# Kernel optimization log

Hardware: AMD Instinct MI355X
Metric: run time of the kernel (lower is better)

The kernel has to match this reference:

```python
import jax, jax.numpy as jnp
import numpy as np

HEADS = 4
F_OUT = 64
NEG_SLOPE = 0.2


def setup_inputs() -> dict:
    key = jax.random.key(0)
    k1, k2, k3, k4 = jax.random.split(key, 4)
    N, F_IN = 4096, 256
    x = jax.random.normal(k1, (N, F_IN), dtype=jnp.float32)
    adj = jax.random.randint(k2, (N, N), 0, 2, dtype=jnp.int32)
    # nn.Linear stores weight [out, in]; we store transposed [in, out] for x @ W
    W = jax.random.normal(k3, (F_IN, F_OUT * HEADS), dtype=jnp.float32) * (1.0 / np.sqrt(F_IN))
    a = jax.random.normal(k4, (2 * F_OUT, 1), dtype=jnp.float32) * 0.1
    return {"x": x, "adj": adj, "W": W, "a": a}


def reference(x, adj, W, a):
    N = x.shape[0]
    h = (x @ W).reshape(N, HEADS, F_OUT)              # [N, H, F]
    # matmul(cat(h_i, h_j), a) == h_i @ a1 + h_j @ a2 (exact, avoids O(N^2*2F) h_cat)
    a1 = a[:F_OUT, 0]
    a2 = a[F_OUT:, 0]
    e_i = jnp.einsum('nhf,f->nh', h, a1)              # [N, H]
    e_j = jnp.einsum('nhf,f->nh', h, a2)              # [N, H]
    e = e_i[:, None, :] + e_j[None, :, :]             # [N, N, H]
    e = jnp.where(e > 0, e, NEG_SLOPE * e)            # LeakyReLU(0.2)
    e = jnp.where(adj[:, :, None] == 0, -jnp.inf, e)
    attention = jax.nn.softmax(e, axis=1)             # softmax over source nodes j
    h_prime = jnp.einsum('ijh,jhf->ihf', attention, h)  # [N, H, F]
    return h_prime.mean(axis=1)                       # heads > 1 -> mean over heads
```

## Files before the change

kernel.cpp:

```cpp
#include <hip/hip_runtime.h>

#define N     4096
#define FIN   256
#define CC    256
#define HEADS 4
#define FOUT  64
#define XPITCH 266

typedef __attribute__((ext_vector_type(8))) short bf16x8;
typedef __attribute__((ext_vector_type(4))) float f32x4;
typedef __attribute__((ext_vector_type(2))) float f32x2;

__device__ inline unsigned cvtpk(float lo, float hi) {
    unsigned r;
    asm("v_cvt_pk_bf16_f32 %0, %1, %2" : "=v"(r) : "v"(lo), "v"(hi));
    return r;
}
__device__ inline f32x2 pkmul(f32x2 a, f32x2 b) {
    f32x2 r;
    asm("v_pk_mul_f32 %0, %1, %2" : "=v"(r) : "v"(a), "v"(b));
    return r;
}

__global__ __launch_bounds__(512) void gat_k1a(const float* __restrict__ x,
                                               const float* __restrict__ W,
                                               const float* __restrict__ a,
                                               short* __restrict__ hF,
                                               float2* __restrict__ e1f,
                                               float2* __restrict__ e2f) {
    __shared__ __align__(16) short xs[64][XPITCH];
    __shared__ __align__(16) short wts[64][XPITCH];
    __shared__ __align__(16) short hbuf[64][74];
    const int t    = threadIdx.x;
    const int bid  = blockIdx.x;
    const int lane = t & 63;
    const int w    = t >> 6;

    const int hd = bid >> 6;
    const int n0 = (bid & 63) * 64;
    const int c0 = hd * 64;

    {
        const float4* xsrc = (const float4*)(x + (size_t)n0 * FIN);
        #pragma unroll
        for (int it = 0; it < 8; ++it) {
            const int fi = it * 512 + t;
            const float4 v = xsrc[fi];
            uint2 o;
            o.x = cvtpk(v.x, v.y);
            o.y = cvtpk(v.z, v.w);
            *(uint2*)&xs[fi >> 6][(fi & 63) * 4] = o;
        }
    }
    {
        const int c  = t & 63;
        const int k4 = (t >> 6) * 4;
        #pragma unroll
        for (int it = 0; it < 8; ++it) {
            const int k = it * 32 + k4;
            const float w0 = W[(k + 0) * CC + c0 + c];
            const float w1 = W[(k + 1) * CC + c0 + c];
            const float w2 = W[(k + 2) * CC + c0 + c];
            const float w3 = W[(k + 3) * CC + c0 + c];
            uint2 o;
            o.x = cvtpk(w0, w1);
            o.y = cvtpk(w2, w3);
            *(uint2*)&wts[c][k] = o;
        }
    }
    __syncthreads();

    const int m = lane & 15;
    const int q = lane >> 4;

    if (w < 4) {
        f32x4 acc[4];
        #pragma unroll
        for (int ct = 0; ct < 4; ++ct) acc[ct] = (f32x4){0.f, 0.f, 0.f, 0.f};

        #pragma unroll
        for (int ks = 0; ks < 8; ++ks) {
            const bf16x8 af = *(const bf16x8*)&xs[w * 16 + m][ks * 32 + q * 8];
            #pragma unroll
            for (int ct = 0; ct < 4; ++ct) {
                const bf16x8 bf_ = *(const bf16x8*)&wts[ct * 16 + m][ks * 32 + q * 8];
                acc[ct] = __builtin_amdgcn_mfma_f32_16x16x32_bf16(af, bf_, acc[ct], 0, 0, 0);
            }
        }

        const float a1v[4] = {a[m], a[16 + m], a[32 + m], a[48 + m]};
        const float a2v[4] = {a[64 + m], a[80 + m], a[96 + m], a[112 + m]};
        #pragma unroll
        for (int r = 0; r < 4; ++r) {
            float s1 = 0.f, s2 = 0.f;
            #pragma unroll
            for (int ct = 0; ct < 4; ++ct) {
                s1 = fmaf(acc[ct][r], a1v[ct], s1);
                s2 = fmaf(acc[ct][r], a2v[ct], s2);
            }
            #pragma unroll
            for (int sh = 1; sh < 16; sh <<= 1) {
                s1 += __shfl_xor(s1, sh, 64);
                s2 += __shfl_xor(s2, sh, 64);
            }
            if (m == 0) {
                const int n = n0 + w * 16 + q * 4 + r;
                e1f[(size_t)hd * N + n] = make_float2(__expf(s1), __expf(0.2f * s1));
                e2f[(size_t)hd * N + n] = make_float2(__expf(s2), __expf(0.2f * s2));
            }
        }

        #pragma unroll
        for (int ct = 0; ct < 4; ++ct) {
            const unsigned lo = cvtpk(acc[ct][0], acc[ct][1]);
            const unsigned hi = cvtpk(acc[ct][2], acc[ct][3]);
            unsigned* hp = (unsigned*)&hbuf[ct * 16 + m][w * 16 + q * 4];
            hp[0] = lo;
            hp[1] = hi;
        }
    }
    __syncthreads();

    {
        const int lp = t & 63;
        const int ft = (t >> 6) & 3;
        const int c2 = t >> 8;
        const int mm = lp & 15;
        const int qq = lp >> 4;
        const bf16x8 hv = *(const bf16x8*)&hbuf[ft * 16 + mm][c2 * 32 + qq * 8];
        const size_t jc = (size_t)(n0 >> 5) + c2;
        *(bf16x8*)(hF + ((((size_t)hd * 128 + jc) * 4 + ft) * 64 + lp) * 8) = hv;
    }
}

__global__ __launch_bounds__(256) void gat_k1b(const int* __restrict__ adj,
                                               unsigned* __restrict__ adjb) {
    const int t    = threadIdx.x;
    const int lane = t & 63;
    const int w    = t >> 6;
    const int row  = blockIdx.x * 2 + (w >> 1);
    const int half = w & 1;
    const int4* arow4 = (const int4*)(adj + (size_t)row * N) + half * 512;
    unsigned*   drow  = adjb + (size_t)row * 128 + half * 64;

    int4 ca[8];
    #pragma unroll
    for (int k = 0; k < 8; ++k)
        ca[k] = arow4[k * 64 + lane];
    #pragma unroll
    for (int k = 0; k < 8; ++k) {
        const int4 v = ca[k];
        unsigned n = (v.x != 0 ? 1u : 0u) | (v.y != 0 ? 2u : 0u) |
                     (v.z != 0 ? 4u : 0u) | (v.w != 0 ? 8u : 0u);
        unsigned b  = n   | ((unsigned)__shfl_xor((int)n,   1, 64) << 4);
        unsigned hw = b   | ((unsigned)__shfl_xor((int)b,   2, 64) << 8);
        unsigned d  = hw  | ((unsigned)__shfl_xor((int)hw,  4, 64) << 16);
        if ((lane & 7) == 0) drow[k * 8 + (lane >> 3)] = d;
    }
}

__global__ __launch_bounds__(512, 4) void gat_k2b(const short* __restrict__ hF,
                                                  const unsigned* __restrict__ adjb,
                                                  const float2* __restrict__ e1f,
                                                  const float2* __restrict__ e2f,
                                                  float* __restrict__ num,
                                                  float* __restrict__ Zp) {
    __shared__ __align__(16) short    hstage[2][4096];
    __shared__ __align__(16) float    e2s[2048];
    __shared__ __align__(16) unsigned adjl[128 * 36];
    __shared__ __align__(16) uint4    mtab[256];
    const int t    = threadIdx.x;
    const int lane = t & 63;
    const int g    = t >> 6;
    const int bid  = blockIdx.x;
    const int xcd  = bid & 7;
    const int idx  = bid >> 3;
    const int hd   = idx & 3;
    const int jc   = (idx >> 2) & 3;
    const int it   = xcd | ((idx >> 4) << 3);
    const int i0   = it * 128;
    const int j0   = jc * 1024;
    const int m    = lane & 15;
    const int q    = lane >> 4;
    const int slice = hd * 4 + jc;

    ((float4*)e2s)[t] = ((const float4*)(e2f + (size_t)hd * N + j0))[t];
    {
        const int row = t >> 2, part = t & 3;
        const uint4* src = (const uint4*)(adjb + (size_t)(i0 + row) * 128 + jc * 32 + part * 8);
        uint4* dst = (uint4*)(adjl + row * 36 + part * 8);
        dst[0] = src[0];
        dst[1] = src[1];
    }
    if (t < 256) {
        const unsigned b = t;
        uint4 e;
        e.x = ((b & 1u)   ? 0xFFFFu : 0u) | ((b & 2u)   ? 0xFFFF0000u : 0u);
        e.y = ((b & 4u)   ? 0xFFFFu : 0u) | ((b & 8u)   ? 0xFFFF0000u : 0u);
        e.z = ((b & 16u)  ? 0xFFFFu : 0u) | ((b & 32u)  ? 0xFFFF0000u : 0u);
        e.w = ((b & 64u)  ? 0xFFFFu : 0u) | ((b & 128u) ? 0xFFFF0000u : 0u);
        mtab[b] = e;
    }
    const uint4* gsrc = (const uint4*)(hF + ((size_t)hd * 128 + jc * 32) * 2048);
    ((uint4*)hstage[0])[t] = gsrc[t];
    __syncthreads();

    const int    rowi = i0 + g * 16 + m;
    const float2 E1r  = e1f[(size_t)hd * N + rowi];
    const f32x2  E1pk = (f32x2){E1r.x, E1r.y};

    bf16x8 onesb;
    #pragma unroll
    for (int e = 0; e < 8; ++e) onesb[e] = (short)0x3F80;

    f32x4 acc[4];
    #pragma unroll
    for (int ft = 0; ft < 4; ++ft) acc[ft] = (f32x4){0.f, 0.f, 0.f, 0.f};
    f32x4 accz = (f32x4){0.f, 0.f, 0.f, 0.f};

    const unsigned char* ab = ((const unsigned char*)adjl) + (g * 16 + m) * 144 + q;

    int cur = 0;
    #pragma unroll 2
    for (int mac = 0; mac < 16; ++mac) {
        const uint4 v = gsrc[(size_t)((mac + 1) & 15) * 512 + t];

        const unsigned bits0 = (unsigned)ab[(mac * 2 + 0) * 4];
        const unsigned bits1 = (unsigned)ab[(mac * 2 + 1) * 4];
        const uint4 mk0 = mtab[bits0];
        const uint4 mk1 = mtab[bits1];

        const short* hb = &hstage[cur][0];
        #pragma unroll
        for (int s = 0; s < 2; ++s) {
            const int jloc = mac * 64 + s * 32 + q * 8;
            const bf16x8 b0 = *(const bf16x8*)(hb + s * 2048 + 0 * 512 + lane * 8);
            const bf16x8 b1 = *(const bf16x8*)(hb + s * 2048 + 1 * 512 + lane * 8);
            const bf16x8 b2 = *(const bf16x8*)(hb + s * 2048 + 2 * 512 + lane * 8);
            const bf16x8 b3 = *(const bf16x8*)(hb + s * 2048 + 3 * 512 + lane * 8);
            const float4* ev = (const float4*)&e2s[2 * jloc];
            const float4 d0 = ev[0], d1 = ev[1], d2 = ev[2], d3 = ev[3];
            const uint4 mk = s ? mk1 : mk0;

            const f32x2 p0 = pkmul(E1pk, (f32x2){d0.x, d0.y});
            const f32x2 p1 = pkmul(E1pk, (f32x2){d0.z, d0.w});
            const f32x2 p2 = pkmul(E1pk, (f32x2){d1.x, d1.y});
            const f32x2 p3 = pkmul(E1pk, (f32x2){d1.z, d1.w});
            const f32x2 p4 = pkmul(E1pk, (f32x2){d2.x, d2.y});
            const f32x2 p5 = pkmul(E1pk, (f32x2){d2.z, d2.w});
            const f32x2 p6 = pkmul(E1pk, (f32x2){d3.x, d3.y});
            const f32x2 p7 = pkmul(E1pk, (f32x2){d3.z, d3.w});

            uint4 afu;
            afu.x = cvtpk(fmaxf(p0[0], p0[1]), fmaxf(p1[0], p1[1])) & mk.x;
            afu.y = cvtpk(fmaxf(p2[0], p2[1]), fmaxf(p3[0], p3[1])) & mk.y;
            afu.z = cvtpk(fmaxf(p4[0], p4[1]), fmaxf(p5[0], p5[1])) & mk.z;
            afu.w = cvtpk(fmaxf(p6[0], p6[1]), fmaxf(p7[0], p7[1])) & mk.w;
            const bf16x8 af = __builtin_bit_cast(bf16x8, afu);

            acc[0] = __builtin_amdgcn_mfma_f32_16x16x32_bf16(af, b0, acc[0], 0, 0, 0);
            acc[1] = __builtin_amdgcn_mfma_f32_16x16x32_bf16(af, b1, acc[1], 0, 0, 0);
            acc[2] = __builtin_amdgcn_mfma_f32_16x16x32_bf16(af, b2, acc[2], 0, 0, 0);
            acc[3] = __builtin_amdgcn_mfma_f32_16x16x32_bf16(af, b3, acc[3], 0, 0, 0);
            accz   = __builtin_amdgcn_mfma_f32_16x16x32_bf16(af, onesb, accz, 0, 0, 0);
        }

        if (mac < 15) {
            ((uint4*)hstage[cur ^ 1])[t] = v;
            __syncthreads();
            cur ^= 1;
        }
    }

    if (m == 0) {
        #pragma unroll
        for (int r = 0; r < 4; ++r)
            Zp[(size_t)slice * N + i0 + g * 16 + q * 4 + r] = accz[r];
    }

    {
        float* nrow = num + ((size_t)slice * N + i0 + g * 16) * FOUT;
        #pragma unroll
        for (int ft = 0; ft < 4; ++ft)
            #pragma unroll
            for (int r = 0; r < 4; ++r)
                nrow[(q * 4 + r) * FOUT + ft * 16 + m] = acc[ft][r];
    }
}

__global__ __launch_bounds__(256) void gat_k3(const float* __restrict__ num,
                                              const float* __restrict__ Zp,
                                              float* __restrict__ out) {
    const int g4 = blockIdx.x * 256 + threadIdx.x;
    const int i  = g4 >> 4;
    const int fo = (g4 & 15) * 4;
    float4 r = make_float4(0.f, 0.f, 0.f, 0.f);
    #pragma unroll
    for (int hd = 0; hd < 4; ++hd) {
        float4 s = make_float4(0.f, 0.f, 0.f, 0.f);
        float  z = 0.f;
        #pragma unroll
        for (int jc = 0; jc < 4; ++jc) {
            const int sl = hd * 4 + jc;
            const float4 v = *(const float4*)(num + ((size_t)sl * N + i) * FOUT + fo);
            s.x += v.x; s.y += v.y; s.z += v.z; s.w += v.w;
            z += Zp[(size_t)sl * N + i];
        }
        const float inv = 1.f / z;
        r.x += s.x * inv; r.y += s.y * inv; r.z += s.z * inv; r.w += s.w * inv;
    }
    r.x *= 0.25f; r.y *= 0.25f; r.z *= 0.25f; r.w *= 0.25f;
    *(float4*)(out + (size_t)i * FOUT + fo) = r;
}

extern "C" void kernel_launch(void* const* d_in, const int* in_sizes, int n_in,
                              void* d_out, int out_size, void* d_ws, size_t ws_size,
                              hipStream_t stream) {
    const float* x   = (const float*)d_in[0];
    const int*   adj = (const int*)d_in[1];
    const float* W   = (const float*)d_in[2];
    const float* a   = (const float*)d_in[3];
    float* out = (float*)d_out;

    short*    hF   = (short*)d_ws;
    float2*   e1f  = (float2*)(hF + (size_t)HEADS * FOUT * N);
    float2*   e2f  = e1f + (size_t)HEADS * N;
    unsigned* adjb = (unsigned*)(e2f + (size_t)HEADS * N);
    float*    num  = (float*)(adjb + (size_t)N * 128);
    float*    Zp   = num + (size_t)16 * N * FOUT;

    gat_k1a<<<256, 512, 0, stream>>>(x, W, a, hF, e1f, e2f);
    gat_k1b<<<2048, 256, 0, stream>>>(adj, adjb);
    gat_k2b<<<512, 512, 0, stream>>>(hF, adjb, e1f, e2f, num, Zp);
    gat_k3<<<256, 256, 0, stream>>>(num, Zp, out);
}
```

Before: 132.6 us.

## Double rows per wave in attention matmul kernel and compute masks inline

Each wave of the attention-aggregation kernel now handles 32 destination rows instead of 16. Every B-fragment of h loaded from LDS feeds two MFMA row tiles, and the grid is halved to 256 blocks. The LDS lookup table for adjacency masks is removed; masks are built per element with shift and arithmetic-shift ops instead. In exchange, register pressure roughly doubles for the accumulators, the min-blocks launch bound is dropped, and only 256 blocks launch, which may leave compute units underfilled.

```diff
diff --git a/kernel.cpp b/kernel.cpp
--- a/kernel.cpp
+++ b/kernel.cpp
@@ -159,16 +159,15 @@
     }
 }
 
-__global__ __launch_bounds__(512, 4) void gat_k2b(const short* __restrict__ hF,
-                                                  const unsigned* __restrict__ adjb,
-                                                  const float2* __restrict__ e1f,
-                                                  const float2* __restrict__ e2f,
-                                                  float* __restrict__ num,
-                                                  float* __restrict__ Zp) {
+__global__ __launch_bounds__(512) void gat_k2b(const short* __restrict__ hF,
+                                               const unsigned* __restrict__ adjb,
+                                               const float2* __restrict__ e1f,
+                                               const float2* __restrict__ e2f,
+                                               float* __restrict__ num,
+                                               float* __restrict__ Zp) {
     __shared__ __align__(16) short    hstage[2][4096];
     __shared__ __align__(16) float    e2s[2048];
-    __shared__ __align__(16) unsigned adjl[128 * 36];
-    __shared__ __align__(16) uint4    mtab[256];
+    __shared__ __align__(16) unsigned adjl[256 * 36];
     const int t    = threadIdx.x;
     const int lane = t & 63;
     const int g    = t >> 6;
@@ -178,7 +177,7 @@
     const int hd   = idx & 3;
     const int jc   = (idx >> 2) & 3;
     const int it   = xcd | ((idx >> 4) << 3);
-    const int i0   = it * 128;
+    const int i0   = it * 256;
     const int j0   = jc * 1024;
     const int m    = lane & 15;
     const int q    = lane >> 4;
@@ -186,49 +185,42 @@
 
     ((float4*)e2s)[t] = ((const float4*)(e2f + (size_t)hd * N + j0))[t];
     {
-        const int row = t >> 2, part = t & 3;
-        const uint4* src = (const uint4*)(adjb + (size_t)(i0 + row) * 128 + jc * 32 + part * 8);
-        uint4* dst = (uint4*)(adjl + row * 36 + part * 8);
-        dst[0] = src[0];
-        dst[1] = src[1];
-    }
-    if (t < 256) {
-        const unsigned b = t;
-        uint4 e;
-        e.x = ((b & 1u)   ? 0xFFFFu : 0u) | ((b & 2u)   ? 0xFFFF0000u : 0u);
-        e.y = ((b & 4u)   ? 0xFFFFu : 0u) | ((b & 8u)   ? 0xFFFF0000u : 0u);
-        e.z = ((b & 16u)  ? 0xFFFFu : 0u) | ((b & 32u)  ? 0xFFFF0000u : 0u);
-        e.w = ((b & 64u)  ? 0xFFFFu : 0u) | ((b & 128u) ? 0xFFFF0000u : 0u);
-        mtab[b] = e;
+        const int row = t >> 1;
+        const int p0  = (t & 1) * 4;
+        const uint4* src = (const uint4*)(adjb + (size_t)(i0 + row) * 128 + jc * 32);
+        uint4* dst = (uint4*)(adjl + row * 36);
+        #pragma unroll
+        for (int k = 0; k < 4; ++k) dst[p0 + k] = src[p0 + k];
     }
     const uint4* gsrc = (const uint4*)(hF + ((size_t)hd * 128 + jc * 32) * 2048);
     ((uint4*)hstage[0])[t] = gsrc[t];
     __syncthreads();
 
-    const int    rowi = i0 + g * 16 + m;
-    const float2 E1r  = e1f[(size_t)hd * N + rowi];
-    const f32x2  E1pk = (f32x2){E1r.x, E1r.y};
+    const int    ra   = i0 + g * 32 + m;
+    const float2 E1a  = e1f[(size_t)hd * N + ra];
+    const float2 E1b  = e1f[(size_t)hd * N + ra + 16];
+    const f32x2  E1pa = (f32x2){E1a.x, E1a.y};
+    const f32x2  E1pb = (f32x2){E1b.x, E1b.y};
 
     bf16x8 onesb;
     #pragma unroll
     for (int e = 0; e < 8; ++e) onesb[e] = (short)0x3F80;
 
-    f32x4 acc[4];
-    #pragma unroll
-    for (int ft = 0; ft < 4; ++ft) acc[ft] = (f32x4){0.f, 0.f, 0.f, 0.f};
-    f32x4 accz = (f32x4){0.f, 0.f, 0.f, 0.f};
-
-    const unsigned char* ab = ((const unsigned char*)adjl) + (g * 16 + m) * 144 + q;
+    f32x4 accf[4], accg[4];
+    #pragma unroll
+    for (int ft = 0; ft < 4; ++ft) {
+        accf[ft] = (f32x4){0.f, 0.f, 0.f, 0.f};
+        accg[ft] = (f32x4){0.f, 0.f, 0.f, 0.f};
+    }
+    f32x4 acczf = (f32x4){0.f, 0.f, 0.f, 0.f};
+    f32x4 acczg = (f32x4){0.f, 0.f, 0.f, 0.f};
+
+    const unsigned char* aba = ((const unsigned char*)adjl) + (g * 32 + m) * 144 + q;
+    const unsigned char* abb = aba + 16 * 144;
 
     int cur = 0;
-    #pragma unroll 2
     for (int mac = 0; mac < 16; ++mac) {
         const uint4 v = gsrc[(size_t)((mac + 1) & 15) * 512 + t];
-
-        const unsigned bits0 = (unsigned)ab[(mac * 2 + 0) * 4];
-        const unsigned bits1 = (unsigned)ab[(mac * 2 + 1) * 4];
-        const uint4 mk0 = mtab[bits0];
-        const uint4 mk1 = mtab[bits1];
 
         const short* hb = &hstage[cur][0];
         #pragma unroll
@@ -240,29 +232,43 @@
             const bf16x8 b3 = *(const bf16x8*)(hb + s * 2048 + 3 * 512 + lane * 8);
             const float4* ev = (const float4*)&e2s[2 * jloc];
             const float4 d0 = ev[0], d1 = ev[1], d2 = ev[2], d3 = ev[3];
-            const uint4 mk = s ? mk1 : mk0;
-
-            const f32x2 p0 = pkmul(E1pk, (f32x2){d0.x, d0.y});
-            const f32x2 p1 = pkmul(E1pk, (f32x2){d0.z, d0.w});
-            const f32x2 p2 = pkmul(E1pk, (f32x2){d1.x, d1.y});
-            const f32x2 p3 = pkmul(E1pk, (f32x2){d1.z, d1.w});
-            const f32x2 p4 = pkmul(E1pk, (f32x2){d2.x, d2.y});
-            const f32x2 p5 = pkmul(E1pk, (f32x2){d2.z, d2.w});
-            const f32x2 p6 = pkmul(E1pk, (f32x2){d3.x, d3.y});
-            const f32x2 p7 = pkmul(E1pk, (f32x2){d3.z, d3.w});
-
-            uint4 afu;
-            afu.x = cvtpk(fmaxf(p0[0], p0[1]), fmaxf(p1[0], p1[1])) & mk.x;
-            afu.y = cvtpk(fmaxf(p2[0], p2[1]), fmaxf(p3[0], p3[1])) & mk.y;
-            afu.z = cvtpk(fmaxf(p4[0], p4[1]), fmaxf(p5[0], p5[1])) & mk.z;
-            afu.w = cvtpk(fmaxf(p6[0], p6[1]), fmaxf(p7[0], p7[1])) & mk.w;
-            const bf16x8 af = __builtin_bit_cast(bf16x8, afu);
-
-            acc[0] = __builtin_amdgcn_mfma_f32_16x16x32_bf16(af, b0, acc[0], 0, 0, 0);
-            acc[1] = __builtin_amdgcn_mfma_f32_16x16x32_bf16(af, b1, acc[1], 0, 0, 0);
-            acc[2] = __builtin_amdgcn_mfma_f32_16x16x32_bf16(af, b2, acc[2], 0, 0, 0);
-            acc[3] = __builtin_amdgcn_mfma_f32_16x16x32_bf16(af, b3, acc[3], 0, 0, 0);
-            accz   = __builtin_amdgcn_mfma_f32_16x16x32_bf16(af, onesb, accz, 0, 0, 0);
+            const unsigned bitsa = (unsigned)aba[(mac * 2 + s) * 4];
+            const unsigned bitsb = (unsigned)abb[(mac * 2 + s) * 4];
+
+            const float ep[8] = {d0.x, d0.z, d1.x, d1.z, d2.x, d2.z, d3.x, d3.z};
+            const float en[8] = {d0.y, d0.w, d1.y, d1.w, d2.y, d2.w, d3.y, d3.w};
+
+            float wa[8], wb[8];
+            #pragma unroll
+            for (int jj = 0; jj < 8; ++jj) {
+                const f32x2 e2j = (f32x2){ep[jj], en[jj]};
+                const f32x2 pa = pkmul(E1pa, e2j);
+                const f32x2 pb = pkmul(E1pb, e2j);
+                const unsigned mka = (unsigned)(((int)(bitsa << (31 - jj))) >> 31);
+                const unsigned mkb = (unsigned)(((int)(bitsb << (31 - jj))) >> 31);
+                float va_ = fmaxf(pa[0], pa[1]);
+                float vb_ = fmaxf(pb[0], pb[1]);
+                wa[jj] = __builtin_bit_cast(float, __builtin_bit_cast(unsigned, va_) & mka);
+                wb[jj] = __builtin_bit_cast(float, __builtin_bit_cast(unsigned, vb_) & mkb);
+            }
+            uint4 au, bu;
+            au.x = cvtpk(wa[0], wa[1]); au.y = cvtpk(wa[2], wa[3]);
+            au.z = cvtpk(wa[4], wa[5]); au.w = cvtpk(wa[6], wa[7]);
+            bu.x = cvtpk(wb[0], wb[1]); bu.y = cvtpk(wb[2], wb[3]);
+            bu.z = cvtpk(wb[4], wb[5]); bu.w = cvtpk(wb[6], wb[7]);
+            const bf16x8 af0 = __builtin_bit_cast(bf16x8, au);
+            const bf16x8 af1 = __builtin_bit_cast(bf16x8, bu);
+
+            accf[0] = __builtin_amdgcn_mfma_f32_16x16x32_bf16(af0, b0, accf[0], 0, 0, 0);
+            accg[0] = __builtin_amdgcn_mfma_f32_16x16x32_bf16(af1, b0, accg[0], 0, 0, 0);
+            accf[1] = __builtin_amdgcn_mfma_f32_16x16x32_bf16(af0, b1, accf[1], 0, 0, 0);
+            accg[1] = __builtin_amdgcn_mfma_f32_16x16x32_bf16(af1, b1, accg[1], 0, 0, 0);
+            accf[2] = __builtin_amdgcn_mfma_f32_16x16x32_bf16(af0, b2, accf[2], 0, 0, 0);
+            accg[2] = __builtin_amdgcn_mfma_f32_16x16x32_bf16(af1, b2, accg[2], 0, 0, 0);
+            accf[3] = __builtin_amdgcn_mfma_f32_16x16x32_bf16(af0, b3, accf[3], 0, 0, 0);
+            accg[3] = __builtin_amdgcn_mfma_f32_16x16x32_bf16(af1, b3, accg[3], 0, 0, 0);
+            acczf   = __builtin_amdgcn_mfma_f32_16x16x32_bf16(af0, onesb, acczf, 0, 0, 0);
+            acczg   = __builtin_amdgcn_mfma_f32_16x16x32_bf16(af1, onesb, acczg, 0, 0, 0);
         }
 
         if (mac < 15) {
@@ -274,17 +280,21 @@
 
     if (m == 0) {
         #pragma unroll
-        for (int r = 0; r < 4; ++r)
-            Zp[(size_t)slice * N + i0 + g * 16 + q * 4 + r] = accz[r];
-    }
-
-    {
-        float* nrow = num + ((size_t)slice * N + i0 + g * 16) * FOUT;
+        for (int r = 0; r < 4; ++r) {
+            Zp[(size_t)slice * N + i0 + g * 32 + q * 4 + r]      = acczf[r];
+            Zp[(size_t)slice * N + i0 + g * 32 + 16 + q * 4 + r] = acczg[r];
+        }
+    }
+
+    {
+        float* nrow = num + ((size_t)slice * N + i0 + g * 32) * FOUT;
         #pragma unroll
         for (int ft = 0; ft < 4; ++ft)
             #pragma unroll
-            for (int r = 0; r < 4; ++r)
-                nrow[(q * 4 + r) * FOUT + ft * 16 + m] = acc[ft][r];
+            for (int r = 0; r < 4; ++r) {
+                nrow[(q * 4 + r) * FOUT + ft * 16 + m]        = accf[ft][r];
+                nrow[(16 + q * 4 + r) * FOUT + ft * 16 + m]   = accg[ft][r];
+            }
     }
 }
 
@@ -331,6 +341,6 @@
 
     gat_k1a<<<256, 512, 0, stream>>>(x, W, a, hF, e1f, e2f);
     gat_k1b<<<2048, 256, 0, stream>>>(adj, adjb);
-    gat_k2b<<<512, 512, 0, stream>>>(hF, adjb, e1f, e2f, num, Zp);
+    gat_k2b<<<256, 512, 0, stream>>>(hF, adjb, e1f, e2f, num, Zp);
     gat_k3<<<256, 256, 0, stream>>>(num, Zp, out);
 }
```

Result: slower. 139.9 us (+5.5%).
